# Performance work log

Measured on AMD Instinct MI355X. Metric: run time of the kernel, lower is better.

Reference implementation:

```python
import jax, jax.numpy as jnp
import numpy as np

N = 32768        # nodes
E = 524288       # edges (avg degree 16)
F_NODE = 64      # NODE_FEATURE_DIM
H = 128          # GNN_HIDDEN
F_EDGE = 32      # EDGE_FEATURE_DIM
L = 3            # GNN_LAYERS
D = 256          # D_MODEL
B = 64           # graphs per batch
MAXN = N // B    # 512 nodes per graph (equal-size for static to_dense_batch)


def setup_inputs() -> dict:
    key = jax.random.key(0)
    ks = jax.random.split(key, 10)
    p = lambda k, shape: jax.random.normal(k, shape, jnp.float32) * 0.02
    return {
        "x": jax.random.normal(ks[0], (N, F_NODE), jnp.float32),
        "edge_attr": jax.random.normal(ks[1], (E, F_EDGE), jnp.float32),
        "node_emb_w": p(ks[2], (F_NODE, H)), "node_emb_b": jnp.zeros((H,), jnp.float32),
        "msg_w1": p(ks[3], (L, 2 * H + F_EDGE, 2 * H)), "msg_b1": jnp.zeros((L, 2 * H), jnp.float32),
        "msg_w2": p(ks[4], (L, 2 * H, H)), "msg_b2": jnp.zeros((L, H), jnp.float32),
        "upd_w": p(ks[5], (L, 2 * H, H)), "upd_b": jnp.zeros((L, H), jnp.float32),
        "upd_ln_g": jnp.ones((L, H), jnp.float32), "upd_ln_b": jnp.zeros((L, H), jnp.float32),
        "norm_g": jnp.ones((L, H), jnp.float32), "norm_b": jnp.zeros((L, H), jnp.float32),
        "proj_w": p(ks[6], (H, D)), "proj_b": jnp.zeros((D,), jnp.float32),
        "edge_index": jax.random.randint(ks[7], (2, E), 0, N),
        "batch": jnp.arange(N, dtype=jnp.int32) // MAXN,  # sorted, 64 graphs of 512
    }


def layer_norm(x, g, b, eps=1e-5):
    m = x.mean(-1, keepdims=True)
    v = ((x - m) ** 2).mean(-1, keepdims=True)
    return (x - m) * jax.lax.rsqrt(v + eps) * g + b


def reference(x, edge_attr, node_emb_w, node_emb_b, msg_w1, msg_b1, msg_w2, msg_b2,
              upd_w, upd_b, upd_ln_g, upd_ln_b, norm_g, norm_b, proj_w, proj_b,
              edge_index, batch):
    src, dst = edge_index[0], edge_index[1]  # PyG: x_j = x[src], x_i = x[dst]
    h = x @ node_emb_w + node_emb_b          # [N, H]
    n_layers = msg_w1.shape[0]
    for l in range(n_layers):
        # message: gather -> concat -> MLP (dropout inactive at eval)
        m = jnp.concatenate([h[dst], h[src], edge_attr], axis=-1)  # [E, 2H+Fe]
        m = jax.nn.relu(m @ msg_w1[l] + msg_b1[l])
        m = m @ msg_w2[l] + msg_b2[l]                               # [E, H]
        # aggregate: scatter-add over destination nodes
        aggr = jax.ops.segment_sum(m, dst, num_segments=h.shape[0])  # [N, H]
        # update: concat -> Linear -> ReLU -> LayerNorm
        u = jnp.concatenate([h, aggr], axis=-1) @ upd_w[l] + upd_b[l]
        u = layer_norm(jax.nn.relu(u), upd_ln_g[l], upd_ln_b[l])
        # residual + outer LayerNorm
        h = layer_norm(h + u, norm_g[l], norm_b[l])
    # to_dense_batch (batch sorted, equal-size graphs -> static [B, MAXN])
    n = h.shape[0]
    counts = jax.ops.segment_sum(jnp.ones((n,), jnp.int32), batch, num_segments=B)
    starts = jnp.concatenate([jnp.zeros((1,), jnp.int32), jnp.cumsum(counts)[:-1]])
    pos = jnp.arange(n, dtype=jnp.int32) - starts[batch]
    dense = jnp.zeros((B, MAXN, h.shape[-1]), h.dtype).at[batch, pos].set(h)
    mask = jnp.zeros((B, MAXN), bool).at[batch, pos].set(True)
    return dense @ proj_w + proj_b, mask
```

## Files before the change

### kernel.cpp

```cpp
#include <hip/hip_runtime.h>

#define NN 32768
#define NE 524288

typedef __attribute__((ext_vector_type(8))) short bf16x8;
typedef __attribute__((ext_vector_type(4))) float f32x4;

__device__ __forceinline__ unsigned short f2bf(float f) {
  unsigned int u = __float_as_uint(f);
  unsigned int r = (u + 0x7FFFu + ((u >> 16) & 1u)) >> 16;
  return (unsigned short)r;
}
__device__ __forceinline__ float bf2f(unsigned short s) {
  return __uint_as_float(((unsigned int)s) << 16);
}

__device__ __forceinline__ void lds_fence_wave() {
  asm volatile("s_waitcnt lgkmcnt(0)" ::: "memory");
  __builtin_amdgcn_sched_barrier(0);
}

__global__ void prep_frag_kernel(const float* __restrict__ W, int row0, int ldw, long lstrW,
                                 unsigned short* __restrict__ out, int outOff, int outLstr,
                                 int K, int N, int total) {
  int t = blockIdx.x * 256 + threadIdx.x;
  if (t >= total) return;
  int lane = t & 63, fi = t >> 6;
  int FR = (K >> 5) * (N >> 4);
  int l = fi / FR; fi -= l * FR;
  int NT = N >> 4;
  int nt = fi % NT, kc = fi / NT;
  int i = lane & 15, g = lane >> 4;
  const float* base = W + (long)l * lstrW;
  bf16x8 v;
#pragma unroll
  for (int j = 0; j < 8; ++j)
    v[j] = (short)f2bf(base[(long)(row0 + kc * 32 + g * 8 + j) * ldw + nt * 16 + i]);
  reinterpret_cast<bf16x8*>(out)[(long)(l * outLstr + outOff + fi) * 64 + lane] = v;
}

__global__ void wcomp_kernel(const float* __restrict__ W2, const float* __restrict__ Wu,
                             float* __restrict__ out) {
  int t = blockIdx.x * 256 + threadIdx.x;
  if (t >= 3 * 256 * 128) return;
  int c = t & 127, a = (t >> 7) & 255, l = t >> 15;
  const float* w2 = W2 + (long)l * 32768 + a * 128;
  const float* wu = Wu + (long)l * 32768 + 128 * 128 + c;
  float s = 0.f;
#pragma unroll 8
  for (int j = 0; j < 128; ++j) s += w2[j] * wu[j * 128];
  out[t] = s;
}

__global__ void c2_kernel(const float* __restrict__ b2, const float* __restrict__ Wu,
                          float* __restrict__ out) {
  int t = blockIdx.x * 256 + threadIdx.x;
  if (t >= 3 * 128) return;
  int c = t & 127, l = t >> 7;
  const float* bb = b2 + l * 128;
  const float* wu = Wu + (long)l * 32768 + 128 * 128 + c;
  float s = 0.f;
#pragma unroll 8
  for (int j = 0; j < 128; ++j) s += bb[j] * wu[j * 128];
  out[t] = s;
}

__global__ void hist_kernel(const int* __restrict__ eidx, int* __restrict__ deg) {
  int t = blockIdx.x * 256 + threadIdx.x;
  if (t < NE) atomicAdd(&deg[eidx[NE + t]], 1);
}

__global__ void scan_kernel(const int* __restrict__ deg, int* __restrict__ cursor,
                            float* __restrict__ degf) {
  __shared__ int lds[1024];
  int t = threadIdx.x;
  int vals[32];
  int s = 0;
#pragma unroll
  for (int j = 0; j < 32; ++j) {
    int d = deg[t * 32 + j];
    vals[j] = d; s += d;
    degf[t * 32 + j] = (float)d;
  }
  lds[t] = s;
  __syncthreads();
  for (int off = 1; off < 1024; off <<= 1) {
    int tmp = 0;
    if (t >= off) tmp = lds[t - off];
    __syncthreads();
    lds[t] += tmp;
    __syncthreads();
  }
  int run = lds[t] - s;
#pragma unroll
  for (int j = 0; j < 32; ++j) { cursor[t * 32 + j] = run; run += vals[j]; }
}

__global__ void scatter_kernel(const int* __restrict__ eidx, const float* __restrict__ ea,
                               int* __restrict__ cursor,
                               int* __restrict__ dsts, int* __restrict__ srcs,
                               unsigned short* __restrict__ ea_s) {
  int t = blockIdx.x * 256 + threadIdx.x;
  if (t >= NE) return;
  int d = eidx[NE + t], s = eidx[t];
  int pos = atomicAdd(&cursor[d], 1);
  dsts[pos] = d;
  srcs[pos] = s;
  const float4* ep = reinterpret_cast<const float4*>(ea + (long)t * 32);
  unsigned short* op = ea_s + (long)pos * 32;
#pragma unroll
  for (int q = 0; q < 4; ++q) {
    float4 f0 = ep[2 * q], f1 = ep[2 * q + 1];
    bf16x8 v;
    v[0] = (short)f2bf(f0.x); v[1] = (short)f2bf(f0.y);
    v[2] = (short)f2bf(f0.z); v[3] = (short)f2bf(f0.w);
    v[4] = (short)f2bf(f1.x); v[5] = (short)f2bf(f1.y);
    v[6] = (short)f2bf(f1.z); v[7] = (short)f2bf(f1.w);
    *reinterpret_cast<bf16x8*>(op + q * 8) = v;
  }
}

__global__ __launch_bounds__(256, 2)
void node_emb_kernel(const float* __restrict__ x,
                     const unsigned short* __restrict__ wf,
                     const float* __restrict__ bias,
                     unsigned short* __restrict__ h_bf,
                     float* __restrict__ h_f32) {
  int tid = threadIdx.x, lane = tid & 63, w = tid >> 6;
  int i = lane & 15, g = lane >> 4;
  int nbase = blockIdx.x * 64 + w * 16;
  f32x4 zero = {0.f, 0.f, 0.f, 0.f};
  f32x4 acc[8];
#pragma unroll
  for (int nt = 0; nt < 8; ++nt) acc[nt] = zero;
#pragma unroll
  for (int kc = 0; kc < 2; ++kc) {
    const float* xp = x + (nbase + i) * 64 + kc * 32 + g * 8;
    float4 f0 = *reinterpret_cast<const float4*>(xp);
    float4 f1 = *reinterpret_cast<const float4*>(xp + 4);
    bf16x8 af;
    af[0] = (short)f2bf(f0.x); af[1] = (short)f2bf(f0.y);
    af[2] = (short)f2bf(f0.z); af[3] = (short)f2bf(f0.w);
    af[4] = (short)f2bf(f1.x); af[5] = (short)f2bf(f1.y);
    af[6] = (short)f2bf(f1.z); af[7] = (short)f2bf(f1.w);
#pragma unroll
    for (int nt = 0; nt < 8; ++nt) {
      bf16x8 bf = reinterpret_cast<const bf16x8*>(wf)[(kc * 8 + nt) * 64 + lane];
      acc[nt] = __builtin_amdgcn_mfma_f32_16x16x32_bf16(af, bf, acc[nt], 0, 0, 0);
    }
  }
#pragma unroll
  for (int nt = 0; nt < 8; ++nt) {
    int c = nt * 16 + i;
    float b = bias[c];
#pragma unroll
    for (int r = 0; r < 4; ++r) {
      int node = nbase + 4 * g + r;
      float v = acc[nt][r] + b;
      h_f32[node * 128 + c] = v;
      h_bf[node * 128 + c] = f2bf(v);
    }
  }
}

__global__ __launch_bounds__(256, 2)
void pq_kernel(const unsigned short* __restrict__ h_bf,
               const unsigned short* __restrict__ wfa,
               const unsigned short* __restrict__ wfb,
               const float* __restrict__ b1,
               unsigned short* __restrict__ P, unsigned short* __restrict__ Q) {
  int tid = threadIdx.x, lane = tid & 63, w = tid >> 6;
  int i = lane & 15, g = lane >> 4;
  int nbase = blockIdx.x * 64 + w * 16;
  f32x4 zero = {0.f, 0.f, 0.f, 0.f};
  f32x4 accP[16], accQ[16];
#pragma unroll
  for (int nt = 0; nt < 16; ++nt) { accP[nt] = zero; accQ[nt] = zero; }
#pragma unroll
  for (int kc = 0; kc < 4; ++kc) {
    bf16x8 af = *reinterpret_cast<const bf16x8*>(h_bf + (nbase + i) * 128 + kc * 32 + g * 8);
#pragma unroll
    for (int nt = 0; nt < 16; ++nt) {
      bf16x8 ba = reinterpret_cast<const bf16x8*>(wfa)[(kc * 16 + nt) * 64 + lane];
      accP[nt] = __builtin_amdgcn_mfma_f32_16x16x32_bf16(af, ba, accP[nt], 0, 0, 0);
      bf16x8 bb = reinterpret_cast<const bf16x8*>(wfb)[(kc * 16 + nt) * 64 + lane];
      accQ[nt] = __builtin_amdgcn_mfma_f32_16x16x32_bf16(af, bb, accQ[nt], 0, 0, 0);
    }
  }
#pragma unroll
  for (int nt = 0; nt < 16; ++nt) {
    int c = nt * 16 + i;
    float b = b1[c];
#pragma unroll
    for (int r = 0; r < 4; ++r) {
      int node = nbase + 4 * g + r;
      P[(long)node * 256 + c] = f2bf(accP[nt][r] + b);
      Q[(long)node * 256 + c] = f2bf(accQ[nt][r]);
    }
  }
}

#define RP 264
__global__ __launch_bounds__(128, 4)
void edge_kernel4(const unsigned short* __restrict__ P,
                  const unsigned short* __restrict__ Q,
                  const int* __restrict__ dsts, const int* __restrict__ srcs,
                  const unsigned short* __restrict__ ea_s,
                  const unsigned short* __restrict__ w1cf,
                  float* __restrict__ haggr) {
  __shared__ unsigned short R[32 * RP];
  __shared__ int dsl[32], ssl[32];
  __shared__ float xch[2][256];
  const int tid = threadIdx.x;
  const int lane = tid & 63, w = tid >> 6;
  const int i = lane & 15, g = lane >> 4;
  const int p0 = blockIdx.x * 32;
  const int kb = w * 16;

  if (lane < 16) {
    dsl[kb + lane] = dsts[p0 + kb + lane];
    ssl[kb + lane] = srcs[p0 + kb + lane];
  }

  {
    bf16x8 bfrag = *reinterpret_cast<const bf16x8*>(ea_s + (long)(p0 + kb + i) * 32 + g * 8);
    f32x4 zero = {0.f, 0.f, 0.f, 0.f};
    f32x4 acc[16];
#pragma unroll
    for (int m = 0; m < 16; ++m) acc[m] = zero;
#pragma unroll
    for (int m = 0; m < 16; ++m) {
      bf16x8 afrag = reinterpret_cast<const bf16x8*>(w1cf)[m * 64 + lane];
      acc[m] = __builtin_amdgcn_mfma_f32_16x16x32_bf16(afrag, bfrag, acc[m], 0, 0, 0);
    }
#pragma unroll
    for (int m = 0; m < 16; ++m) {
      union { unsigned short s[4]; unsigned long long u; } pk;
#pragma unroll
      for (int r = 0; r < 4; ++r) pk.s[r] = f2bf(acc[m][r]);
      *reinterpret_cast<unsigned long long*>(&R[(kb + i) * RP + m * 16 + 4 * g]) = pk.u;
    }
  }
  lds_fence_wave();

  const int c4 = lane * 4;
  float acc4[4] = {0.f, 0.f, 0.f, 0.f};
  int dvPrev = dsl[kb];
  float pf[4];
  {
    ushort4 pv = *reinterpret_cast<const ushort4*>(P + (long)dvPrev * 256 + c4);
    pf[0] = bf2f(pv.x); pf[1] = bf2f(pv.y); pf[2] = bf2f(pv.z); pf[3] = bf2f(pv.w);
  }

#pragma unroll
  for (int k = 0; k < 16; ++k) {
    int pos = kb + k;
    int dv = dsl[pos], sv = ssl[pos];
    if (dv != dvPrev) {
      *reinterpret_cast<float4*>(&xch[w][c4]) = make_float4(acc4[0], acc4[1], acc4[2], acc4[3]);
      lds_fence_wave();
      float* hp = haggr + (long)dvPrev * 256;
#pragma unroll
      for (int j = 0; j < 4; ++j) atomicAdd(hp + lane + 64 * j, xch[w][lane + 64 * j]);
      acc4[0] = acc4[1] = acc4[2] = acc4[3] = 0.f;
      ushort4 pv = *reinterpret_cast<const ushort4*>(P + (long)dv * 256 + c4);
      pf[0] = bf2f(pv.x); pf[1] = bf2f(pv.y); pf[2] = bf2f(pv.z); pf[3] = bf2f(pv.w);
      dvPrev = dv;
    }
    ushort4 qv = *reinterpret_cast<const ushort4*>(Q + (long)sv * 256 + c4);
    ushort4 rv = *reinterpret_cast<const ushort4*>(&R[pos * RP + c4]);
    float v0 = pf[0] + bf2f(qv.x) + bf2f(rv.x);
    float v1 = pf[1] + bf2f(qv.y) + bf2f(rv.y);
    float v2 = pf[2] + bf2f(qv.z) + bf2f(rv.z);
    float v3 = pf[3] + bf2f(qv.w) + bf2f(rv.w);
    acc4[0] += v0 > 0.f ? v0 : 0.f;
    acc4[1] += v1 > 0.f ? v1 : 0.f;
    acc4[2] += v2 > 0.f ? v2 : 0.f;
    acc4[3] += v3 > 0.f ? v3 : 0.f;
  }
  {
    *reinterpret_cast<float4*>(&xch[w][c4]) = make_float4(acc4[0], acc4[1], acc4[2], acc4[3]);
    lds_fence_wave();
    float* hp = haggr + (long)dvPrev * 256;
#pragma unroll
    for (int j = 0; j < 4; ++j) atomicAdd(hp + lane + 64 * j, xch[w][lane + 64 * j]);
  }
}

__global__ __launch_bounds__(256, 2)
void upd_kernel2(const unsigned short* __restrict__ h_bf_in,
                 float* __restrict__ h_f32,
                 const float* __restrict__ haggr,
                 const float* __restrict__ degf,
                 const unsigned short* __restrict__ wf,
                 const float* __restrict__ ub, const float* __restrict__ c2,
                 const float* __restrict__ g1, const float* __restrict__ be1,
                 const float* __restrict__ g2, const float* __restrict__ be2,
                 unsigned short* __restrict__ h_bf_out) {
  int tid = threadIdx.x, lane = tid & 63, w = tid >> 6;
  int i = lane & 15, g = lane >> 4;
  int nbase = blockIdx.x * 64 + w * 16;
  f32x4 zero = {0.f, 0.f, 0.f, 0.f};
  f32x4 acc[8];
#pragma unroll
  for (int nt = 0; nt < 8; ++nt) acc[nt] = zero;
#pragma unroll
  for (int kc = 0; kc < 12; ++kc) {
    bf16x8 af;
    if (kc < 4) {
      af = *reinterpret_cast<const bf16x8*>(h_bf_in + (nbase + i) * 128 + kc * 32 + g * 8);
    } else {
      const float* ap = haggr + (long)(nbase + i) * 256 + (kc - 4) * 32 + g * 8;
      float4 f0 = *reinterpret_cast<const float4*>(ap);
      float4 f1 = *reinterpret_cast<const float4*>(ap + 4);
      af[0] = (short)f2bf(f0.x); af[1] = (short)f2bf(f0.y);
      af[2] = (short)f2bf(f0.z); af[3] = (short)f2bf(f0.w);
      af[4] = (short)f2bf(f1.x); af[5] = (short)f2bf(f1.y);
      af[6] = (short)f2bf(f1.z); af[7] = (short)f2bf(f1.w);
    }
#pragma unroll
    for (int nt = 0; nt < 8; ++nt) {
      bf16x8 bf = reinterpret_cast<const bf16x8*>(wf)[(kc * 8 + nt) * 64 + lane];
      acc[nt] = __builtin_amdgcn_mfma_f32_16x16x32_bf16(af, bf, acc[nt], 0, 0, 0);
    }
  }
  float vv[8][4];
#pragma unroll
  for (int nt = 0; nt < 8; ++nt) {
    int c = nt * 16 + i;
    float b = ub[c], cc = c2[c];
#pragma unroll
    for (int r = 0; r < 4; ++r) {
      int node = nbase + 4 * g + r;
      float t = acc[nt][r] + b + degf[node] * cc;
      vv[nt][r] = t > 0.f ? t : 0.f;
    }
  }
#pragma unroll
  for (int r = 0; r < 4; ++r) {
    float s = 0.f, s2 = 0.f;
#pragma unroll
    for (int nt = 0; nt < 8; ++nt) { s += vv[nt][r]; s2 += vv[nt][r] * vv[nt][r]; }
#pragma unroll
    for (int mk = 1; mk < 16; mk <<= 1) { s += __shfl_xor(s, mk, 64); s2 += __shfl_xor(s2, mk, 64); }
    float mean = s * (1.f / 128.f);
    float var = s2 * (1.f / 128.f) - mean * mean;
    float inv = rsqrtf(var + 1e-5f);
    int node = nbase + 4 * g + r;
    float tv[8];
    float sb = 0.f, sb2 = 0.f;
#pragma unroll
    for (int nt = 0; nt < 8; ++nt) {
      int c = nt * 16 + i;
      float u = (vv[nt][r] - mean) * inv * g1[c] + be1[c];
      float t = h_f32[node * 128 + c] + u;
      tv[nt] = t;
      sb += t; sb2 += t * t;
    }
#pragma unroll
    for (int mk = 1; mk < 16; mk <<= 1) { sb += __shfl_xor(sb, mk, 64); sb2 += __shfl_xor(sb2, mk, 64); }
    float mean2 = sb * (1.f / 128.f);
    float var2 = sb2 * (1.f / 128.f) - mean2 * mean2;
    float inv2 = rsqrtf(var2 + 1e-5f);
#pragma unroll
    for (int nt = 0; nt < 8; ++nt) {
      int c = nt * 16 + i;
      float o = (tv[nt] - mean2) * inv2 * g2[c] + be2[c];
      h_f32[node * 128 + c] = o;
      h_bf_out[node * 128 + c] = f2bf(o);
    }
  }
}

__global__ __launch_bounds__(256, 2)
void proj_kernel(const unsigned short* __restrict__ h_bf,
                 const unsigned short* __restrict__ wf,
                 const float* __restrict__ bias,
                 float* __restrict__ out, float* __restrict__ mask) {
  int tid = threadIdx.x, lane = tid & 63, w = tid >> 6;
  int i = lane & 15, g = lane >> 4;
  int nbase = blockIdx.x * 64 + w * 16;
  if (tid < 64) mask[blockIdx.x * 64 + tid] = 1.0f;
  f32x4 zero = {0.f, 0.f, 0.f, 0.f};
  f32x4 acc[16];
#pragma unroll
  for (int nt = 0; nt < 16; ++nt) acc[nt] = zero;
#pragma unroll
  for (int kc = 0; kc < 4; ++kc) {
    bf16x8 af = *reinterpret_cast<const bf16x8*>(h_bf + (nbase + i) * 128 + kc * 32 + g * 8);
#pragma unroll
    for (int nt = 0; nt < 16; ++nt) {
      bf16x8 bf = reinterpret_cast<const bf16x8*>(wf)[(kc * 16 + nt) * 64 + lane];
      acc[nt] = __builtin_amdgcn_mfma_f32_16x16x32_bf16(af, bf, acc[nt], 0, 0, 0);
    }
  }
#pragma unroll
  for (int nt = 0; nt < 16; ++nt) {
    int c = nt * 16 + i;
    float b = bias[c];
#pragma unroll
    for (int r = 0; r < 4; ++r) {
      int node = nbase + 4 * g + r;
      out[(long)node * 256 + c] = acc[nt][r] + b;
    }
  }
}

extern "C" void kernel_launch(void* const* d_in, const int* in_sizes, int n_in,
                              void* d_out, int out_size, void* d_ws, size_t ws_size,
                              hipStream_t stream) {
  const float* x      = (const float*)d_in[0];
  const float* ea     = (const float*)d_in[1];
  const float* emb_w  = (const float*)d_in[2];
  const float* emb_b  = (const float*)d_in[3];
  const float* msg_w1 = (const float*)d_in[4];
  const float* msg_b1 = (const float*)d_in[5];
  const float* msg_w2 = (const float*)d_in[6];
  const float* msg_b2 = (const float*)d_in[7];
  const float* upd_w  = (const float*)d_in[8];
  const float* upd_b  = (const float*)d_in[9];
  const float* uln_g  = (const float*)d_in[10];
  const float* uln_b  = (const float*)d_in[11];
  const float* nrm_g  = (const float*)d_in[12];
  const float* nrm_b  = (const float*)d_in[13];
  const float* proj_w = (const float*)d_in[14];
  const float* proj_b = (const float*)d_in[15];
  const int*   eidx   = (const int*)d_in[16];

  char* ws = (char*)d_ws;
  size_t off = 0;
  auto take = [&](size_t b) { char* p = ws + off; off = (off + b + 255) & ~(size_t)255; return p; };
  unsigned short* h_bf  = (unsigned short*)take((size_t)NN * 128 * 2);
  float*          h_f32 = (float*)take((size_t)NN * 128 * 4);
  unsigned short* Pb    = (unsigned short*)take((size_t)NN * 256 * 2);
  unsigned short* Qb    = (unsigned short*)take((size_t)NN * 256 * 2);
  float*          haggr = (float*)take((size_t)NN * 256 * 4);
  unsigned short* ea_s  = (unsigned short*)take((size_t)NE * 32 * 2);
  int*            dsts  = (int*)take((size_t)NE * 4);
  int*            srcs  = (int*)take((size_t)NE * 4);
  int*            deg   = (int*)take((size_t)NN * 4);
  int*            cursor= (int*)take((size_t)NN * 4);
  float*          degf  = (float*)take((size_t)NN * 4);
  float*          wcomp = (float*)take((size_t)3 * 256 * 128 * 4);
  float*          c2b   = (float*)take((size_t)3 * 128 * 4);
  unsigned short* wembf = (unsigned short*)take((size_t)16 * 64 * 8 * 2);
  unsigned short* w1af  = (unsigned short*)take((size_t)3 * 64 * 64 * 8 * 2);
  unsigned short* w1bf  = (unsigned short*)take((size_t)3 * 64 * 64 * 8 * 2);
  unsigned short* w1cf  = (unsigned short*)take((size_t)3 * 16 * 64 * 8 * 2);
  unsigned short* wupdf = (unsigned short*)take((size_t)3 * 96 * 64 * 8 * 2);
  unsigned short* wprojf= (unsigned short*)take((size_t)64 * 64 * 8 * 2);
  (void)ws_size; (void)n_in; (void)in_sizes;

  hipMemsetAsync(deg, 0, (size_t)NN * 4, stream);
  hist_kernel<<<2048, 256, 0, stream>>>(eidx, deg);
  scan_kernel<<<1, 1024, 0, stream>>>(deg, cursor, degf);
  scatter_kernel<<<2048, 256, 0, stream>>>(eidx, ea, cursor, dsts, srcs, ea_s);
  wcomp_kernel<<<384, 256, 0, stream>>>(msg_w2, upd_w, wcomp);
  c2_kernel<<<2, 256, 0, stream>>>(msg_b2, upd_w, c2b);
  prep_frag_kernel<<<4, 256, 0, stream>>>(emb_w, 0, 128, 0, wembf, 0, 16, 64, 128, 1024);
  prep_frag_kernel<<<48, 256, 0, stream>>>(msg_w1, 0, 256, 73728, w1af, 0, 64, 128, 256, 12288);
  prep_frag_kernel<<<48, 256, 0, stream>>>(msg_w1, 128, 256, 73728, w1bf, 0, 64, 128, 256, 12288);
  prep_frag_kernel<<<12, 256, 0, stream>>>(msg_w1, 256, 256, 73728, w1cf, 0, 16, 32, 256, 3072);
  prep_frag_kernel<<<24, 256, 0, stream>>>(upd_w, 0, 128, 32768, wupdf, 0, 96, 128, 128, 6144);
  prep_frag_kernel<<<48, 256, 0, stream>>>(wcomp, 0, 128, 32768, wupdf, 32, 96, 256, 128, 12288);
  prep_frag_kernel<<<16, 256, 0, stream>>>(proj_w, 0, 256, 0, wprojf, 0, 64, 128, 256, 4096);

  node_emb_kernel<<<512, 256, 0, stream>>>(x, wembf, emb_b, h_bf, h_f32);

  for (int l = 0; l < 3; ++l) {
    hipMemsetAsync(haggr, 0, (size_t)NN * 256 * 4, stream);
    pq_kernel<<<512, 256, 0, stream>>>(h_bf, w1af + (size_t)l * 32768, w1bf + (size_t)l * 32768,
                                       msg_b1 + l * 256, Pb, Qb);
    edge_kernel4<<<NE / 32, 128, 0, stream>>>(Pb, Qb, dsts, srcs, ea_s,
                                              w1cf + (size_t)l * 8192, haggr);
    upd_kernel2<<<512, 256, 0, stream>>>(h_bf, h_f32, haggr, degf,
                                         wupdf + (size_t)l * 49152, upd_b + l * 128,
                                         c2b + l * 128,
                                         uln_g + l * 128, uln_b + l * 128,
                                         nrm_g + l * 128, nrm_b + l * 128, h_bf);
  }

  proj_kernel<<<512, 256, 0, stream>>>(h_bf, wprojf, proj_b, (float*)d_out,
                                       (float*)d_out + (size_t)NN * 256);
}
```

Baseline: 541.8 us.

## Fold aggregate zeroing into pq kernel and prefetch edge gathers into registers

The per-layer memset of the aggregation buffer is removed, and each pq_kernel block now zeros its own 64-node slice of haggr. In the edge kernel, destination and source indices become wave-uniform scalar loads instead of LDS staging, and all 16 Q-row gathers are issued up front into registers before the LDS fence. The aim is to drop a memset launch and overlap gather latency with the edge-feature MFMA work. The cost is higher register pressure from the 16 prefetched vectors, which could reduce occupancy.

Measured after the change: 505.3 us. 6.7% less time.

```diff
diff --git a/kernel.cpp b/kernel.cpp
--- a/kernel.cpp
+++ b/kernel.cpp
@@ -168,10 +168,17 @@
                const unsigned short* __restrict__ wfa,
                const unsigned short* __restrict__ wfb,
                const float* __restrict__ b1,
-               unsigned short* __restrict__ P, unsigned short* __restrict__ Q) {
+               unsigned short* __restrict__ P, unsigned short* __restrict__ Q,
+               float* __restrict__ haggr) {
   int tid = threadIdx.x, lane = tid & 63, w = tid >> 6;
   int i = lane & 15, g = lane >> 4;
   int nbase = blockIdx.x * 64 + w * 16;
+  {
+    const float4 zz = make_float4(0.f, 0.f, 0.f, 0.f);
+    float4* hz = reinterpret_cast<float4*>(haggr + (long)blockIdx.x * 64 * 256);
+#pragma unroll
+    for (int it = 0; it < 16; ++it) hz[tid + 256 * it] = zz;
+  }
   f32x4 zero = {0.f, 0.f, 0.f, 0.f};
   f32x4 accP[16], accQ[16];
 #pragma unroll
@@ -202,14 +209,13 @@
 
 #define RP 264
 __global__ __launch_bounds__(128, 4)
-void edge_kernel4(const unsigned short* __restrict__ P,
+void edge_kernel5(const unsigned short* __restrict__ P,
                   const unsigned short* __restrict__ Q,
                   const int* __restrict__ dsts, const int* __restrict__ srcs,
                   const unsigned short* __restrict__ ea_s,
                   const unsigned short* __restrict__ w1cf,
                   float* __restrict__ haggr) {
   __shared__ unsigned short R[32 * RP];
-  __shared__ int dsl[32], ssl[32];
   __shared__ float xch[2][256];
   const int tid = threadIdx.x;
   const int lane = tid & 63, w = tid >> 6;
@@ -217,9 +223,11 @@
   const int p0 = blockIdx.x * 32;
   const int kb = w * 16;
 
-  if (lane < 16) {
-    dsl[kb + lane] = dsts[p0 + kb + lane];
-    ssl[kb + lane] = srcs[p0 + kb + lane];
+  int dvs[16], svs[16];
+#pragma unroll
+  for (int k = 0; k < 16; ++k) {
+    dvs[k] = __builtin_amdgcn_readfirstlane(dsts[p0 + kb + k]);
+    svs[k] = __builtin_amdgcn_readfirstlane(srcs[p0 + kb + k]);
   }
 
   {
@@ -241,21 +249,25 @@
       *reinterpret_cast<unsigned long long*>(&R[(kb + i) * RP + m * 16 + 4 * g]) = pk.u;
     }
   }
-  lds_fence_wave();
 
   const int c4 = lane * 4;
-  float acc4[4] = {0.f, 0.f, 0.f, 0.f};
-  int dvPrev = dsl[kb];
+  ushort4 qv[16];
+#pragma unroll
+  for (int k = 0; k < 16; ++k)
+    qv[k] = *reinterpret_cast<const ushort4*>(Q + (long)svs[k] * 256 + c4);
   float pf[4];
+  int dvPrev = dvs[0];
   {
     ushort4 pv = *reinterpret_cast<const ushort4*>(P + (long)dvPrev * 256 + c4);
     pf[0] = bf2f(pv.x); pf[1] = bf2f(pv.y); pf[2] = bf2f(pv.z); pf[3] = bf2f(pv.w);
   }
 
+  lds_fence_wave();
+
+  float acc4[4] = {0.f, 0.f, 0.f, 0.f};
 #pragma unroll
   for (int k = 0; k < 16; ++k) {
-    int pos = kb + k;
-    int dv = dsl[pos], sv = ssl[pos];
+    int dv = dvs[k];
     if (dv != dvPrev) {
       *reinterpret_cast<float4*>(&xch[w][c4]) = make_float4(acc4[0], acc4[1], acc4[2], acc4[3]);
       lds_fence_wave();
@@ -267,12 +279,11 @@
       pf[0] = bf2f(pv.x); pf[1] = bf2f(pv.y); pf[2] = bf2f(pv.z); pf[3] = bf2f(pv.w);
       dvPrev = dv;
     }
-    ushort4 qv = *reinterpret_cast<const ushort4*>(Q + (long)sv * 256 + c4);
-    ushort4 rv = *reinterpret_cast<const ushort4*>(&R[pos * RP + c4]);
-    float v0 = pf[0] + bf2f(qv.x) + bf2f(rv.x);
-    float v1 = pf[1] + bf2f(qv.y) + bf2f(rv.y);
-    float v2 = pf[2] + bf2f(qv.z) + bf2f(rv.z);
-    float v3 = pf[3] + bf2f(qv.w) + bf2f(rv.w);
+    ushort4 rv = *reinterpret_cast<const ushort4*>(&R[(kb + k) * RP + c4]);
+    float v0 = pf[0] + bf2f(qv[k].x) + bf2f(rv.x);
+    float v1 = pf[1] + bf2f(qv[k].y) + bf2f(rv.y);
+    float v2 = pf[2] + bf2f(qv[k].z) + bf2f(rv.z);
+    float v3 = pf[3] + bf2f(qv[k].w) + bf2f(rv.w);
     acc4[0] += v0 > 0.f ? v0 : 0.f;
     acc4[1] += v1 > 0.f ? v1 : 0.f;
     acc4[2] += v2 > 0.f ? v2 : 0.f;
@@ -468,10 +479,9 @@
   node_emb_kernel<<<512, 256, 0, stream>>>(x, wembf, emb_b, h_bf, h_f32);
 
   for (int l = 0; l < 3; ++l) {
-    hipMemsetAsync(haggr, 0, (size_t)NN * 256 * 4, stream);
     pq_kernel<<<512, 256, 0, stream>>>(h_bf, w1af + (size_t)l * 32768, w1bf + (size_t)l * 32768,
-                                       msg_b1 + l * 256, Pb, Qb);
-    edge_kernel4<<<NE / 32, 128, 0, stream>>>(Pb, Qb, dsts, srcs, ea_s,
+                                       msg_b1 + l * 256, Pb, Qb, haggr);
+    edge_kernel5<<<NE / 32, 128, 0, stream>>>(Pb, Qb, dsts, srcs, ea_s,
                                               w1cf + (size_t)l * 8192, haggr);
     upd_kernel2<<<512, 256, 0, stream>>>(h_bf, h_f32, haggr, degf,
                                          wupdf + (size_t)l * 49152, upd_b + l * 128,
```
